# Optimization experiments

Measured on AMD Instinct MI355X. Metric: run time of the kernel, lower is better.

Reference implementation:

```python
import jax, jax.numpy as jnp
import numpy as np

WINDOW = 256  # sw_attention_window_size; query i attends to keys j with i-WINDOW <= j <= i


def setup_inputs() -> dict:
    key = jax.random.key(0)
    kq, kk, kv = jax.random.split(key, 3)
    shape = (4, 16, 4096, 64)  # [B, H, S, D]
    q = jax.random.normal(kq, shape, dtype=jnp.float32)
    k = jax.random.normal(kk, shape, dtype=jnp.float32)
    v = jax.random.normal(kv, shape, dtype=jnp.float32)
    return {"q": q, "k": k, "v": v}


def _local_attention(q, k, v, window):
    # Block-banded sliding-window attention: mask (j >= i - window) & (j <= i).
    # Uses block size == window so each query block only needs 2 key blocks.
    b, h, S, d = q.shape
    W = window
    T = S // W  # number of query blocks
    scale = jnp.asarray(d, q.dtype) ** -0.5  # flex_attention default scale

    qb = q.reshape(b, h, T, W, d)  # [b,h,T,W,d]

    def windows(x):
        # pad one block of zeros in front, then each query block t sees
        # key positions [t*W - W, t*W + W) == blocks (t, t+1) of the padded seq
        xp = jnp.pad(x, ((0, 0), (0, 0), (W, 0), (0, 0)))
        blk = xp.reshape(b, h, T + 1, W, d)
        return jnp.concatenate([blk[:, :, :-1], blk[:, :, 1:]], axis=3)  # [b,h,T,2W,d]

    kw = windows(k)
    vw = windows(v)

    # mask: global i = t*W + qi, global j = t*W - W + kj
    qi = jnp.arange(W)[:, None]          # [W,1]
    kj = jnp.arange(2 * W)[None, :]      # [1,2W]
    band = (kj >= qi) & (kj <= qi + W)   # i-W <= j <= i   -> [W,2W]
    t = jnp.arange(T)[:, None, None]     # [T,1,1]
    valid = (t * W - W + kj[None, :, :]) >= 0  # j >= 0 (drop padded keys)
    mask = band[None, :, :] & valid      # [T,W,2W]

    scores = jnp.einsum('bhtqd,bhtkd->bhtqk', qb, kw) * scale  # [b,h,T,W,2W]
    scores = jnp.where(mask[None, None], scores, -jnp.inf)
    attn = jax.nn.softmax(scores, axis=-1)
    out = jnp.einsum('bhtqk,bhtkd->bhtqd', attn, vw)
    return out.reshape(b, h, S, d)


def reference(q, k, v):
    return _local_attention(q, k, v, WINDOW)
```

## Files before the change

kernel.cpp:

```cpp
#include <hip/hip_runtime.h>

typedef __attribute__((ext_vector_type(8))) short bf16x8;
typedef __attribute__((ext_vector_type(4))) float f32x4;

#define L2E 1.44269504088896340736f

__device__ __forceinline__ unsigned f2bf(float x) {
    union { float f; unsigned u; } c; c.f = x;
    return (c.u + 0x7FFFu + ((c.u >> 16) & 1u)) >> 16;
}
__device__ __forceinline__ unsigned pk2(float lo, float hi) {
    return f2bf(lo) | (f2bf(hi) << 16);
}

constexpr int D_   = 64;
constexpr int SEQ  = 4096;
constexpr int MQ   = 128;
constexpr int CK   = 128;
constexpr int KSTR = 72;
constexpr int VSTR = 132;
constexpr int OSTR = 68;

constexpr int SMEM_BYTES = 35840;

__global__ __launch_bounds__(256, 2)
void swattn_kernel(const float* __restrict__ Qg, const float* __restrict__ Kg,
                   const float* __restrict__ Vg, float* __restrict__ Og)
{
    __shared__ __align__(16) char smem[SMEM_BYTES];
    unsigned short* k_lds = (unsigned short*)smem;
    unsigned short* v_lds = (unsigned short*)(smem + CK * KSTR * 2);
    float*          o_lds = (float*)smem;

    const int tid  = threadIdx.x;
    const int wv   = tid >> 6;
    const int lane = tid & 63;
    const int g    = lane >> 4;
    const int n    = lane & 15;

    const int bh = blockIdx.x & 63;
    const int qb = blockIdx.x >> 6;
    const size_t base = (size_t)bh * SEQ * D_;
    const int q0 = qb * MQ;

    bf16x8 qf[2][2];
    #pragma unroll
    for (int nt = 0; nt < 2; ++nt) {
        const float* qp = Qg + base + (size_t)(q0 + wv * 32 + nt * 16 + n) * D_;
        #pragma unroll
        for (int ks = 0; ks < 2; ++ks) {
            f32x4 a = *(const f32x4*)(qp + ks * 32 + g * 8);
            f32x4 b = *(const f32x4*)(qp + ks * 32 + g * 8 + 4);
            union { bf16x8 v; unsigned u[4]; } t;
            t.u[0] = pk2(a.x * 0.125f, a.y * 0.125f);
            t.u[1] = pk2(a.z * 0.125f, a.w * 0.125f);
            t.u[2] = pk2(b.x * 0.125f, b.y * 0.125f);
            t.u[3] = pk2(b.z * 0.125f, b.w * 0.125f);
            qf[nt][ks] = t.v;
        }
    }

    f32x4 o_ac[4][2];
    #pragma unroll
    for (int a = 0; a < 4; ++a)
        #pragma unroll
        for (int b = 0; b < 2; ++b)
            o_ac[a][b] = f32x4{0.f, 0.f, 0.f, 0.f};
    float m_r[2] = {-1e30f, -1e30f};
    float l_r[2] = {0.0f, 0.0f};

    #pragma unroll
    for (int ci = 0; ci < 3; ++ci) {
        const int cb = qb - 2 + ci;
        if (cb < 0) continue;

        __syncthreads();

        {
            const f32x4* kp = (const f32x4*)(Kg + base + (size_t)cb * CK * D_);
            #pragma unroll
            for (int i = 0; i < 8; ++i) {
                int idx = tid + 256 * i;
                int row = idx >> 4, c4 = idx & 15;
                f32x4 x = kp[idx];
                *(uint2*)&k_lds[row * KSTR + c4 * 4] =
                    make_uint2(pk2(x.x, x.y), pk2(x.z, x.w));
            }
        }
        {
            const f32x4* vp = (const f32x4*)(Vg + base + (size_t)cb * CK * D_);
            const int g16 = tid & 15, kq = tid >> 4;
            #pragma unroll
            for (int h = 0; h < 2; ++h) {
                int key0 = (kq + 16 * h) * 4;
                union { f32x4 v; float f[4]; } r0, r1, r2, r3;
                r0.v = vp[(key0 + 0) * 16 + g16];
                r1.v = vp[(key0 + 1) * 16 + g16];
                r2.v = vp[(key0 + 2) * 16 + g16];
                r3.v = vp[(key0 + 3) * 16 + g16];
                #pragma unroll
                for (int i = 0; i < 4; ++i) {
                    *(uint2*)&v_lds[(g16 * 4 + i) * VSTR + key0] =
                        make_uint2(pk2(r0.f[i], r1.f[i]), pk2(r2.f[i], r3.f[i]));
                }
            }
        }
        __syncthreads();

        f32x4 sc[8][2];
        #pragma unroll
        for (int mt = 0; mt < 8; ++mt)
            #pragma unroll
            for (int nt = 0; nt < 2; ++nt)
                sc[mt][nt] = f32x4{0.f, 0.f, 0.f, 0.f};

        #pragma unroll
        for (int ks = 0; ks < 2; ++ks) {
            #pragma unroll
            for (int mt = 0; mt < 8; ++mt) {
                bf16x8 af = *(const bf16x8*)&k_lds[(mt * 16 + n) * KSTR + ks * 32 + g * 8];
                sc[mt][0] = __builtin_amdgcn_mfma_f32_16x16x32_bf16(af, qf[0][ks], sc[mt][0], 0, 0, 0);
                sc[mt][1] = __builtin_amdgcn_mfma_f32_16x16x32_bf16(af, qf[1][ks], sc[mt][1], 0, 0, 0);
            }
        }

        if (ci != 1) {
            #pragma unroll
            for (int mt = 0; mt < 8; ++mt)
                #pragma unroll
                for (int nt = 0; nt < 2; ++nt)
                    #pragma unroll
                    for (int r = 0; r < 4; ++r) {
                        int kk = mt * 16 + g * 4 + r;
                        int qq = wv * 32 + nt * 16 + n;
                        bool ok = (ci == 0) ? (kk >= qq) : (kk <= qq);
                        if (!ok) sc[mt][nt][r] = -1e30f;
                    }
        }

        uint2 pkv[8][2];
        #pragma unroll
        for (int nt = 0; nt < 2; ++nt) {
            float mx = -1e30f;
            #pragma unroll
            for (int mt = 0; mt < 8; ++mt)
                #pragma unroll
                for (int r = 0; r < 4; ++r)
                    mx = fmaxf(mx, sc[mt][nt][r]);
            mx = fmaxf(mx, __shfl_xor(mx, 16, 64));
            mx = fmaxf(mx, __shfl_xor(mx, 32, 64));
            float mnew = fmaxf(m_r[nt], mx);
            float al   = __builtin_amdgcn_exp2f((m_r[nt] - mnew) * L2E);
            m_r[nt] = mnew;
            float c  = -mnew * L2E;
            float rs = 0.f;
            #pragma unroll
            for (int mt = 0; mt < 8; ++mt) {
                #pragma unroll
                for (int r = 0; r < 4; ++r) {
                    float p = __builtin_amdgcn_exp2f(fmaf(sc[mt][nt][r], L2E, c));
                    sc[mt][nt][r] = p;
                    rs += p;
                }
                pkv[mt][nt] = make_uint2(pk2(sc[mt][nt][0], sc[mt][nt][1]),
                                         pk2(sc[mt][nt][2], sc[mt][nt][3]));
            }
            rs += __shfl_xor(rs, 16, 64);
            rs += __shfl_xor(rs, 32, 64);
            l_r[nt] = l_r[nt] * al + rs;
            #pragma unroll
            for (int mtd = 0; mtd < 4; ++mtd)
                #pragma unroll
                for (int r = 0; r < 4; ++r)
                    o_ac[mtd][nt][r] *= al;
        }

        #pragma unroll
        for (int kp4 = 0; kp4 < 4; ++kp4) {
            bf16x8 bfr[2];
            #pragma unroll
            for (int nt = 0; nt < 2; ++nt) {
                union { bf16x8 v; uint2 u2[2]; } bb;
                bb.u2[0] = pkv[2 * kp4][nt];
                bb.u2[1] = pkv[2 * kp4 + 1][nt];
                bfr[nt] = bb.v;
            }
            #pragma unroll
            for (int mtd = 0; mtd < 4; ++mtd) {
                int bus = (mtd * 16 + n) * VSTR + kp4 * 32 + g * 4;
                union { bf16x8 v; uint2 u2[2]; } aa;
                aa.u2[0] = *(const uint2*)&v_lds[bus];
                aa.u2[1] = *(const uint2*)&v_lds[bus + 16];
                o_ac[mtd][0] = __builtin_amdgcn_mfma_f32_16x16x32_bf16(aa.v, bfr[0], o_ac[mtd][0], 0, 0, 0);
                o_ac[mtd][1] = __builtin_amdgcn_mfma_f32_16x16x32_bf16(aa.v, bfr[1], o_ac[mtd][1], 0, 0, 0);
            }
        }
    }

    __syncthreads();
    float inv[2] = {1.0f / l_r[0], 1.0f / l_r[1]};
    #pragma unroll
    for (int mtd = 0; mtd < 4; ++mtd)
        #pragma unroll
        for (int nt = 0; nt < 2; ++nt) {
            f32x4 v = o_ac[mtd][nt];
            v.x *= inv[nt]; v.y *= inv[nt]; v.z *= inv[nt]; v.w *= inv[nt];
            *(f32x4*)&o_lds[(wv * 32 + nt * 16 + n) * OSTR + mtd * 16 + g * 4] = v;
        }
    __syncthreads();

    f32x4* op = (f32x4*)(Og + base + (size_t)q0 * D_);
    #pragma unroll
    for (int p = 0; p < 8; ++p) {
        int row = p * 16 + (tid >> 4);
        int c4  = tid & 15;
        f32x4 v = *(const f32x4*)&o_lds[row * OSTR + c4 * 4];
        op[row * 16 + c4] = v;
    }
}

extern "C" void kernel_launch(void* const* d_in, const int* in_sizes, int n_in,
                              void* d_out, int out_size, void* d_ws, size_t ws_size,
                              hipStream_t stream) {
    (void)in_sizes; (void)n_in; (void)out_size; (void)d_ws; (void)ws_size;
    const float* q = (const float*)d_in[0];
    const float* k = (const float*)d_in[1];
    const float* v = (const float*)d_in[2];
    float* o = (float*)d_out;
    dim3 grid(64 * 32), block(256);
    hipLaunchKernelGGL(swattn_kernel, grid, block, 0, stream, q, k, v, o);
}
```

Baseline: 230.5 us.

## Use hardware bf16 pack, tree reductions, and raise priority around MFMA loops

```diff
diff --git a/kernel.cpp b/kernel.cpp
--- a/kernel.cpp
+++ b/kernel.cpp
@@ -5,12 +5,10 @@
 
 #define L2E 1.44269504088896340736f
 
-__device__ __forceinline__ unsigned f2bf(float x) {
-    union { float f; unsigned u; } c; c.f = x;
-    return (c.u + 0x7FFFu + ((c.u >> 16) & 1u)) >> 16;
-}
 __device__ __forceinline__ unsigned pk2(float lo, float hi) {
-    return f2bf(lo) | (f2bf(hi) << 16);
+    unsigned r;
+    asm("v_cvt_pk_bf16_f32 %0, %1, %2" : "=v"(r) : "v"(lo), "v"(hi));
+    return r;
 }
 
 constexpr int D_   = 64;
@@ -114,6 +112,7 @@
             for (int nt = 0; nt < 2; ++nt)
                 sc[mt][nt] = f32x4{0.f, 0.f, 0.f, 0.f};
 
+        __builtin_amdgcn_s_setprio(1);
         #pragma unroll
         for (int ks = 0; ks < 2; ++ks) {
             #pragma unroll
@@ -123,6 +122,7 @@
                 sc[mt][1] = __builtin_amdgcn_mfma_f32_16x16x32_bf16(af, qf[1][ks], sc[mt][1], 0, 0, 0);
             }
         }
+        __builtin_amdgcn_s_setprio(0);
 
         if (ci != 1) {
             #pragma unroll
@@ -141,30 +141,33 @@
         uint2 pkv[8][2];
         #pragma unroll
         for (int nt = 0; nt < 2; ++nt) {
-            float mx = -1e30f;
+            float t8[8];
             #pragma unroll
             for (int mt = 0; mt < 8; ++mt)
-                #pragma unroll
-                for (int r = 0; r < 4; ++r)
-                    mx = fmaxf(mx, sc[mt][nt][r]);
+                t8[mt] = fmaxf(fmaxf(sc[mt][nt][0], sc[mt][nt][1]),
+                               fmaxf(sc[mt][nt][2], sc[mt][nt][3]));
+            float ma = fmaxf(t8[0], t8[1]), mb = fmaxf(t8[2], t8[3]);
+            float mc = fmaxf(t8[4], t8[5]), md = fmaxf(t8[6], t8[7]);
+            float mx = fmaxf(fmaxf(ma, mb), fmaxf(mc, md));
             mx = fmaxf(mx, __shfl_xor(mx, 16, 64));
             mx = fmaxf(mx, __shfl_xor(mx, 32, 64));
             float mnew = fmaxf(m_r[nt], mx);
             float al   = __builtin_amdgcn_exp2f((m_r[nt] - mnew) * L2E);
             m_r[nt] = mnew;
             float c  = -mnew * L2E;
-            float rs = 0.f;
+            float s8[8];
             #pragma unroll
             for (int mt = 0; mt < 8; ++mt) {
-                #pragma unroll
-                for (int r = 0; r < 4; ++r) {
-                    float p = __builtin_amdgcn_exp2f(fmaf(sc[mt][nt][r], L2E, c));
-                    sc[mt][nt][r] = p;
-                    rs += p;
-                }
-                pkv[mt][nt] = make_uint2(pk2(sc[mt][nt][0], sc[mt][nt][1]),
-                                         pk2(sc[mt][nt][2], sc[mt][nt][3]));
-            }
+                float p0 = __builtin_amdgcn_exp2f(fmaf(sc[mt][nt][0], L2E, c));
+                float p1 = __builtin_amdgcn_exp2f(fmaf(sc[mt][nt][1], L2E, c));
+                float p2 = __builtin_amdgcn_exp2f(fmaf(sc[mt][nt][2], L2E, c));
+                float p3 = __builtin_amdgcn_exp2f(fmaf(sc[mt][nt][3], L2E, c));
+                s8[mt] = (p0 + p1) + (p2 + p3);
+                pkv[mt][nt] = make_uint2(pk2(p0, p1), pk2(p2, p3));
+            }
+            float ra = s8[0] + s8[1], rb = s8[2] + s8[3];
+            float rc = s8[4] + s8[5], rd = s8[6] + s8[7];
+            float rs = (ra + rb) + (rc + rd);
             rs += __shfl_xor(rs, 16, 64);
             rs += __shfl_xor(rs, 32, 64);
             l_r[nt] = l_r[nt] * al + rs;
@@ -175,6 +178,7 @@
                     o_ac[mtd][nt][r] *= al;
         }
 
+        __builtin_amdgcn_s_setprio(1);
         #pragma unroll
         for (int kp4 = 0; kp4 < 4; ++kp4) {
             bf16x8 bfr[2];
@@ -195,6 +199,7 @@
                 o_ac[mtd][1] = __builtin_amdgcn_mfma_f32_16x16x32_bf16(aa.v, bfr[1], o_ac[mtd][1], 0, 0, 0);
             }
         }
+        __builtin_amdgcn_s_setprio(0);
     }
 
     __syncthreads();
```

Result: no change. 230.2 us (-0.1%).
